# Performance work log

Hardware: AMD Instinct MI355X
Metric: run time of the kernel (lower is better)

Reference implementation:

```python
import jax, jax.numpy as jnp
import numpy as np


def _degree_norm(idx, n_nodes):
    # in/out degree, clamped to >=1 (DGL GraphConv behavior), then d^{-1/2}
    deg = jax.ops.segment_sum(jnp.ones(idx.shape[0], jnp.float32), idx,
                              num_segments=n_nodes)
    return jnp.power(jnp.clip(deg, 1.0, None), -0.5)


def _graph_conv(h, src, dst, W, b):
    """DGL GraphConv with norm='both', weight=True, bias=True."""
    n = h.shape[0]
    norm_out = _degree_norm(src, n)  # [N] out-degree^{-1/2} (source side)
    norm_in = _degree_norm(dst, n)   # [N] in-degree^{-1/2} (dest side)
    h = h * norm_out[:, None]
    if W.shape[0] > W.shape[1]:
        # in_feats > out_feats: project first, then aggregate
        h = h @ W
        agg = jax.ops.segment_sum(h[src], dst, num_segments=n)
    else:
        agg = jax.ops.segment_sum(h[src], dst, num_segments=n)
        agg = agg @ W
    return agg * norm_in[:, None] + b


def setup_inputs() -> dict:
    key = jax.random.key(0)
    ks = jax.random.split(key, 6)
    N, E, IN, HID, OUT = 100000, 1600000, 128, 256, 64
    h = jax.random.normal(ks[0], (N, IN), jnp.float32)
    src = jax.random.randint(ks[1], (E,), 0, N, jnp.int32)
    dst = jax.random.randint(ks[2], (E,), 0, N, jnp.int32)
    W1 = jax.random.normal(ks[3], (IN, HID), jnp.float32) * (1.0 / np.sqrt(IN))
    b1 = jnp.zeros((HID,), jnp.float32)
    W2 = jax.random.normal(ks[4], (HID, OUT), jnp.float32) * (1.0 / np.sqrt(HID))
    b2 = jnp.zeros((OUT,), jnp.float32)
    return {"h": h, "src": src, "dst": dst, "W1": W1, "b1": b1,
            "W2": W2, "b2": b2}


def reference(h, src, dst, W1, b1, W2, b2):
    # layer 0: GraphConv -> relu (dropout is identity in eval mode)
    h = _graph_conv(h, src, dst, W1, b1)
    h = jax.nn.relu(h)
    # layer 1 (last): GraphConv only
    h = _graph_conv(h, src, dst, W2, b2)
    return h
```

## Files before the change

### kernel.cpp

```cpp
#include <hip/hip_runtime.h>


__global__ __launch_bounds__(256)
void hist_int(const int* __restrict__ src, const int* __restrict__ dst,
              int* __restrict__ deg_out, int* __restrict__ deg_in, int E)
{
    int e = blockIdx.x * 256 + threadIdx.x;
    if (e < E) {
        atomicAdd(&deg_out[src[e]], 1);
        atomicAdd(&deg_in[dst[e]], 1);
    }
}

__global__ __launch_bounds__(256)
void scan_block_sums(const int* __restrict__ deg, int* __restrict__ blockSums, int N)
{
    int t = threadIdx.x;
    int base = blockIdx.x * 1024 + t * 4;
    int s = 0;
    #pragma unroll
    for (int i = 0; i < 4; ++i) { int idx = base + i; if (idx < N) s += deg[idx]; }
    #pragma unroll
    for (int d = 32; d > 0; d >>= 1) s += __shfl_down(s, d);
    __shared__ int ws[4];
    int wid = t >> 6, lane = t & 63;
    if (lane == 0) ws[wid] = s;
    __syncthreads();
    if (t == 0) blockSums[blockIdx.x] = ws[0] + ws[1] + ws[2] + ws[3];
}

__global__ void scan_offsets(const int* __restrict__ blockSums, int* __restrict__ blockOffs,
                             int NB, int* __restrict__ row_start, int N, int E)
{
    if (threadIdx.x == 0 && blockIdx.x == 0) {
        int run = 0;
        for (int b = 0; b < NB; ++b) { blockOffs[b] = run; run += blockSums[b]; }
        row_start[N] = E;
    }
}

__global__ __launch_bounds__(256)
void scan_write(const int* __restrict__ deg, const int* __restrict__ blockOffs,
                int* __restrict__ row_start, int* __restrict__ cursor, int N)
{
    int t = threadIdx.x, lane = t & 63, wid = t >> 6;
    int base = blockIdx.x * 1024 + t * 4;
    int v[4]; int s = 0;
    #pragma unroll
    for (int i = 0; i < 4; ++i) {
        int idx = base + i;
        v[i] = (idx < N) ? deg[idx] : 0;
        s += v[i];
    }
    int x = s;
    #pragma unroll
    for (int d = 1; d < 64; d <<= 1) { int y = __shfl_up(x, d); if (lane >= d) x += y; }
    __shared__ int wtot[4];
    if (lane == 63) wtot[wid] = x;
    __syncthreads();
    int woff = 0;
    for (int w = 0; w < wid; ++w) woff += wtot[w];
    int run = (x - s) + woff + blockOffs[blockIdx.x];
    #pragma unroll
    for (int i = 0; i < 4; ++i) {
        int idx = base + i;
        if (idx < N) { row_start[idx] = run; cursor[idx] = run; run += v[i]; }
    }
}

__global__ __launch_bounds__(256)
void fill_perm(const int* __restrict__ src, const int* __restrict__ dst,
               int* __restrict__ cursor, int* __restrict__ perm, int E)
{
    int e = blockIdx.x * 256 + threadIdx.x;
    if (e < E) {
        int pos = atomicAdd(&cursor[dst[e]], 1);
        perm[pos] = src[e];
    }
}

__global__ __launch_bounds__(256)
void norm_finalize(int* __restrict__ deg, float* __restrict__ nrm, int n)
{
    int i = blockIdx.x * 256 + threadIdx.x;
    if (i < n) {
        int d = deg[i];
        float df = (float)(d > 1 ? d : 1);
        nrm[i] = 1.0f / sqrtf(df);
    }
}

__global__ __launch_bounds__(256)
void gather_agg128(const float* __restrict__ X, const int* __restrict__ perm,
                   const int* __restrict__ row_start, const float* __restrict__ norm_out,
                   float* __restrict__ out, int N)
{
    int wid = threadIdx.x >> 6, lane = threadIdx.x & 63;
    int n = blockIdx.x * 4 + wid;
    if (n >= N) return;
    int half = lane >> 5;
    int sub  = lane & 31;
    const float4* X4 = (const float4*)X;
    int e = row_start[n], e1 = row_start[n + 1];
    float4 acc = make_float4(0.f, 0.f, 0.f, 0.f);

    for (; e + 4 <= e1; e += 4) {
        int a = perm[e + half];
        int b = perm[e + 2 + half];
        float wa = norm_out[a], wb = norm_out[b];
        float4 va = X4[(size_t)a * 32 + sub];
        float4 vb = X4[(size_t)b * 32 + sub];
        acc.x = fmaf(va.x, wa, fmaf(vb.x, wb, acc.x));
        acc.y = fmaf(va.y, wa, fmaf(vb.y, wb, acc.y));
        acc.z = fmaf(va.z, wa, fmaf(vb.z, wb, acc.z));
        acc.w = fmaf(va.w, wa, fmaf(vb.w, wb, acc.w));
    }
    for (; e + 2 <= e1; e += 2) {
        int a = perm[e + half];
        float wa = norm_out[a];
        float4 va = X4[(size_t)a * 32 + sub];
        acc.x = fmaf(va.x, wa, acc.x);
        acc.y = fmaf(va.y, wa, acc.y);
        acc.z = fmaf(va.z, wa, acc.z);
        acc.w = fmaf(va.w, wa, acc.w);
    }
    if (e < e1 && half == 0) {
        int a = perm[e];
        float wa = norm_out[a];
        float4 va = X4[(size_t)a * 32 + sub];
        acc.x = fmaf(va.x, wa, acc.x);
        acc.y = fmaf(va.y, wa, acc.y);
        acc.z = fmaf(va.z, wa, acc.z);
        acc.w = fmaf(va.w, wa, acc.w);
    }
    acc.x += __shfl_xor(acc.x, 32);
    acc.y += __shfl_xor(acc.y, 32);
    acc.z += __shfl_xor(acc.z, 32);
    acc.w += __shfl_xor(acc.w, 32);
    if (half == 0)
        ((float4*)out)[(size_t)n * 32 + sub] = acc;
}

__global__ __launch_bounds__(256)
void gather_out64(const float* __restrict__ X, const int* __restrict__ perm,
                  const int* __restrict__ row_start, const float* __restrict__ norm_in,
                  const float* __restrict__ bias, float* __restrict__ out, int N)
{
    int wid = threadIdx.x >> 6, lane = threadIdx.x & 63;
    int n = blockIdx.x * 4 + wid;
    if (n >= N) return;
    int q   = lane >> 4;
    int sub = lane & 15;
    const float4* X4 = (const float4*)X;
    int e = row_start[n], e1 = row_start[n + 1];
    float4 acc = make_float4(0.f, 0.f, 0.f, 0.f);

    for (; e + 8 <= e1; e += 8) {
        int a = perm[e + q];
        int b = perm[e + 4 + q];
        float4 va = X4[(size_t)a * 16 + sub];
        float4 vb = X4[(size_t)b * 16 + sub];
        acc.x += va.x + vb.x;
        acc.y += va.y + vb.y;
        acc.z += va.z + vb.z;
        acc.w += va.w + vb.w;
    }
    for (; e + 4 <= e1; e += 4) {
        int a = perm[e + q];
        float4 va = X4[(size_t)a * 16 + sub];
        acc.x += va.x; acc.y += va.y; acc.z += va.z; acc.w += va.w;
    }
    int r = e1 - e;
    if (q < r) {
        int a = perm[e + q];
        float4 va = X4[(size_t)a * 16 + sub];
        acc.x += va.x; acc.y += va.y; acc.z += va.z; acc.w += va.w;
    }
    acc.x += __shfl_xor(acc.x, 32);
    acc.y += __shfl_xor(acc.y, 32);
    acc.z += __shfl_xor(acc.z, 32);
    acc.w += __shfl_xor(acc.w, 32);
    acc.x += __shfl_xor(acc.x, 16);
    acc.y += __shfl_xor(acc.y, 16);
    acc.z += __shfl_xor(acc.z, 16);
    acc.w += __shfl_xor(acc.w, 16);
    if (q == 0) {
        float ni = norm_in[n];
        float4 bv = ((const float4*)bias)[sub];
        float4 o;
        o.x = fmaf(acc.x, ni, bv.x);
        o.y = fmaf(acc.y, ni, bv.y);
        o.z = fmaf(acc.z, ni, bv.z);
        o.w = fmaf(acc.w, ni, bv.w);
        ((float4*)out)[(size_t)n * 16 + sub] = o;
    }
}

template<int BN, int TN, int EPI>
__global__ __launch_bounds__(256)
void gemm_tiled(const float* __restrict__ A, const float* __restrict__ B,
                float* __restrict__ C, int M, int K, int NC,
                const float* __restrict__ norm_in,
                const float* __restrict__ norm_out,
                const float* __restrict__ bias)
{
    __shared__ float As[16][132];
    __shared__ float Bs[16][BN];
    const int tid = threadIdx.x;
    const int tx = tid & 15;
    const int ty = tid >> 4;
    const int brow = blockIdx.x * 128;
    const int bcol = blockIdx.y * BN;

    const int ar = tid >> 2;
    const int ak = (tid & 3) * 4;

    float acc[8][TN] = {};

    for (int k0 = 0; k0 < K; k0 += 16) {
        #pragma unroll
        for (int hh = 0; hh < 2; ++hh) {
            int row = ar + hh * 64;
            int grow = brow + row;
            float4 v = make_float4(0.f, 0.f, 0.f, 0.f);
            if (grow < M) v = *(const float4*)(A + (size_t)grow * K + k0 + ak);
            As[ak + 0][row] = v.x;
            As[ak + 1][row] = v.y;
            As[ak + 2][row] = v.z;
            As[ak + 3][row] = v.w;
        }
        if (BN == 128) {
            #pragma unroll
            for (int hh = 0; hh < 2; ++hh) {
                int kr = (tid >> 5) + hh * 8;
                int cc = (tid & 31) * 4;
                *(float4*)&Bs[kr][cc] =
                    *(const float4*)(B + (size_t)(k0 + kr) * NC + bcol + cc);
            }
        } else {
            int kr = tid >> 4;
            int cc = (tid & 15) * 4;
            *(float4*)&Bs[kr][cc] =
                *(const float4*)(B + (size_t)(k0 + kr) * NC + bcol + cc);
        }
        __syncthreads();
        #pragma unroll
        for (int k = 0; k < 16; ++k) {
            float a0[8], b0[TN];
            *(float4*)&a0[0] = *(const float4*)&As[k][ty * 8];
            *(float4*)&a0[4] = *(const float4*)&As[k][ty * 8 + 4];
            *(float4*)&b0[0] = *(const float4*)&Bs[k][tx * TN];
            if (TN == 8)
                *(float4*)&b0[4] = *(const float4*)&Bs[k][tx * TN + 4];
            #pragma unroll
            for (int i = 0; i < 8; ++i)
                #pragma unroll
                for (int j = 0; j < TN; ++j)
                    acc[i][j] = fmaf(a0[i], b0[j], acc[i][j]);
        }
        __syncthreads();
    }

    #pragma unroll
    for (int i = 0; i < 8; ++i) {
        int row = brow + ty * 8 + i;
        if (row >= M) continue;
        float ni = 0.f, no = 0.f;
        if (EPI == 0) { ni = norm_in[row]; no = norm_out[row]; }
        #pragma unroll
        for (int j4 = 0; j4 < TN; j4 += 4) {
            int col = bcol + tx * TN + j4;
            float4 o = *(float4*)&acc[i][j4];
            if (EPI == 0) {
                o.x = fmaxf(fmaf(o.x, ni, bias[col + 0]), 0.0f) * no;
                o.y = fmaxf(fmaf(o.y, ni, bias[col + 1]), 0.0f) * no;
                o.z = fmaxf(fmaf(o.z, ni, bias[col + 2]), 0.0f) * no;
                o.w = fmaxf(fmaf(o.w, ni, bias[col + 3]), 0.0f) * no;
            }
            *(float4*)(C + (size_t)row * NC + col) = o;
        }
    }
}

extern "C" void kernel_launch(void* const* d_in, const int* in_sizes, int n_in,
                              void* d_out, int out_size, void* d_ws, size_t ws_size,
                              hipStream_t stream)
{
    const float* h   = (const float*)d_in[0];
    const int*   src = (const int*)d_in[1];
    const int*   dst = (const int*)d_in[2];
    const float* W1  = (const float*)d_in[3];
    const float* b1  = (const float*)d_in[4];
    const float* W2  = (const float*)d_in[5];
    const float* b2  = (const float*)d_in[6];
    float* out = (float*)d_out;

    const int HID = in_sizes[4];
    const int OUT = in_sizes[6];
    const int IN  = in_sizes[3] / HID;
    const int N   = in_sizes[0] / IN;
    const int E   = in_sizes[1];
    const int NB  = (N + 1023) / 1024;

    char* p = (char*)d_ws;
    auto alloc = [&](size_t bytes) { void* r = p; p += (bytes + 255) & ~255ULL; return r; };
    int* deg_out   = (int*)alloc((size_t)N * 4);
    int* deg_in    = (int*)alloc((size_t)N * 4);
    int* row_start = (int*)alloc((size_t)(N + 1) * 4);
    int* cursor    = (int*)alloc((size_t)N * 4);
    int* blockSums = (int*)alloc((size_t)NB * 4);
    int* blockOffs = (int*)alloc((size_t)NB * 4);
    int* perm      = (int*)alloc((size_t)E * 4);
    float* agg1    = (float*)alloc((size_t)N * IN * 4);
    float* h1n     = (float*)alloc((size_t)N * HID * 4);
    float* h2      = agg1;
    float* norm_out = (float*)deg_out;
    float* norm_in  = (float*)deg_in;

    hipMemsetAsync(deg_out, 0, (size_t)((char*)row_start - (char*)deg_out), stream);

    hist_int<<<(E + 255) / 256, 256, 0, stream>>>(src, dst, deg_out, deg_in, E);

    scan_block_sums<<<NB, 256, 0, stream>>>(deg_in, blockSums, N);
    scan_offsets<<<1, 64, 0, stream>>>(blockSums, blockOffs, NB, row_start, N, E);
    scan_write<<<NB, 256, 0, stream>>>(deg_in, blockOffs, row_start, cursor, N);

    fill_perm<<<(E + 255) / 256, 256, 0, stream>>>(src, dst, cursor, perm, E);

    norm_finalize<<<(N + 255) / 256, 256, 0, stream>>>(deg_out, norm_out, N);
    norm_finalize<<<(N + 255) / 256, 256, 0, stream>>>(deg_in, norm_in, N);

    gather_agg128<<<(N + 3) / 4, 256, 0, stream>>>(h, perm, row_start, norm_out, agg1, N);

    gemm_tiled<128, 8, 0><<<dim3((N + 127) / 128, HID / 128), 256, 0, stream>>>(
        agg1, W1, h1n, N, IN, HID, norm_in, norm_out, b1);

    gemm_tiled<64, 4, 1><<<dim3((N + 127) / 128, OUT / 64), 256, 0, stream>>>(
        h1n, W2, h2, N, HID, OUT, nullptr, nullptr, nullptr);

    gather_out64<<<(N + 3) / 4, 256, 0, stream>>>(h2, perm, row_start, norm_in, b2, out, N);
}
```

Before: 661.8 us.

## Privatize degree histograms per XCC with workgroup-scope atomics and fuse norm computation

The degree histogram now gives each XCC its own copy, chosen by reading the hardware XCC_ID register. Increments use relaxed workgroup-scope atomics, so they can resolve in that XCC's L2 instead of needing device-wide coherence. A new reduce kernel sums the eight copies, writes deg_in, and computes both normalization vectors, replacing the two norm_finalize launches. The cost is a larger memset and an extra pass over 16N ints stored in the agg1 scratch buffer. Correctness depends on all blocks sharing an XCC using the same L2 for these atomics.

Result: slower. 677.2 us (+2.3%).

```diff
diff --git a/kernel.cpp b/kernel.cpp
--- a/kernel.cpp
+++ b/kernel.cpp
@@ -2,14 +2,40 @@
 
 
 __global__ __launch_bounds__(256)
-void hist_int(const int* __restrict__ src, const int* __restrict__ dst,
-              int* __restrict__ deg_out, int* __restrict__ deg_in, int E)
-{
-    int e = blockIdx.x * 256 + threadIdx.x;
-    if (e < E) {
-        atomicAdd(&deg_out[src[e]], 1);
-        atomicAdd(&deg_in[dst[e]], 1);
-    }
+void hist8_int(const int* __restrict__ src, const int* __restrict__ dst,
+               int* __restrict__ hist_out, int* __restrict__ hist_in,
+               int N, int E)
+{
+    unsigned xcc;
+    asm volatile("s_getreg_b32 %0, hwreg(HW_REG_XCC_ID)" : "=s"(xcc));
+    xcc &= 7;
+    int* ho = hist_out + (size_t)xcc * N;
+    int* hi = hist_in  + (size_t)xcc * N;
+    int stride = gridDim.x * 256;
+    for (int e = blockIdx.x * 256 + threadIdx.x; e < E; e += stride) {
+        __hip_atomic_fetch_add(&ho[src[e]], 1, __ATOMIC_RELAXED,
+                               __HIP_MEMORY_SCOPE_WORKGROUP);
+        __hip_atomic_fetch_add(&hi[dst[e]], 1, __ATOMIC_RELAXED,
+                               __HIP_MEMORY_SCOPE_WORKGROUP);
+    }
+}
+
+__global__ __launch_bounds__(256)
+void reduce_norms(const int* __restrict__ hist_out, const int* __restrict__ hist_in,
+                  int* __restrict__ deg_in, float* __restrict__ norm_out,
+                  float* __restrict__ norm_in, int N)
+{
+    int n = blockIdx.x * 256 + threadIdx.x;
+    if (n >= N) return;
+    int so = 0, si = 0;
+    #pragma unroll
+    for (int c = 0; c < 8; ++c) {
+        so += hist_out[(size_t)c * N + n];
+        si += hist_in[(size_t)c * N + n];
+    }
+    deg_in[n] = si;
+    norm_out[n] = 1.0f / sqrtf((float)(so > 1 ? so : 1));
+    norm_in[n]  = 1.0f / sqrtf((float)(si > 1 ? si : 1));
 }
 
 __global__ __launch_bounds__(256)
@@ -76,17 +102,6 @@
     if (e < E) {
         int pos = atomicAdd(&cursor[dst[e]], 1);
         perm[pos] = src[e];
-    }
-}
-
-__global__ __launch_bounds__(256)
-void norm_finalize(int* __restrict__ deg, float* __restrict__ nrm, int n)
-{
-    int i = blockIdx.x * 256 + threadIdx.x;
-    if (i < n) {
-        int d = deg[i];
-        float df = (float)(d > 1 ? d : 1);
-        nrm[i] = 1.0f / sqrtf(df);
     }
 }
 
@@ -304,7 +319,8 @@
 
     char* p = (char*)d_ws;
     auto alloc = [&](size_t bytes) { void* r = p; p += (bytes + 255) & ~255ULL; return r; };
-    int* deg_out   = (int*)alloc((size_t)N * 4);
+    float* norm_out = (float*)alloc((size_t)N * 4);
+    float* norm_in  = (float*)alloc((size_t)N * 4);
     int* deg_in    = (int*)alloc((size_t)N * 4);
     int* row_start = (int*)alloc((size_t)(N + 1) * 4);
     int* cursor    = (int*)alloc((size_t)N * 4);
@@ -314,12 +330,15 @@
     float* agg1    = (float*)alloc((size_t)N * IN * 4);
     float* h1n     = (float*)alloc((size_t)N * HID * 4);
     float* h2      = agg1;
-    float* norm_out = (float*)deg_out;
-    float* norm_in  = (float*)deg_in;
-
-    hipMemsetAsync(deg_out, 0, (size_t)((char*)row_start - (char*)deg_out), stream);
-
-    hist_int<<<(E + 255) / 256, 256, 0, stream>>>(src, dst, deg_out, deg_in, E);
+
+    int* hist_out8 = (int*)agg1;
+    int* hist_in8  = hist_out8 + 8 * (size_t)N;
+
+    hipMemsetAsync(hist_out8, 0, 16 * (size_t)N * 4, stream);
+
+    hist8_int<<<2048, 256, 0, stream>>>(src, dst, hist_out8, hist_in8, N, E);
+    reduce_norms<<<(N + 255) / 256, 256, 0, stream>>>(
+        hist_out8, hist_in8, deg_in, norm_out, norm_in, N);
 
     scan_block_sums<<<NB, 256, 0, stream>>>(deg_in, blockSums, N);
     scan_offsets<<<1, 64, 0, stream>>>(blockSums, blockOffs, NB, row_start, N, E);
@@ -327,9 +346,6 @@
 
     fill_perm<<<(E + 255) / 256, 256, 0, stream>>>(src, dst, cursor, perm, E);
 
-    norm_finalize<<<(N + 255) / 256, 256, 0, stream>>>(deg_out, norm_out, N);
-    norm_finalize<<<(N + 255) / 256, 256, 0, stream>>>(deg_in, norm_in, N);
-
     gather_agg128<<<(N + 3) / 4, 256, 0, stream>>>(h, perm, row_start, norm_out, agg1, N);
 
     gemm_tiled<128, 8, 0><<<dim3((N + 127) / 128, HID / 128), 256, 0, stream>>>(
```
